# Optimization experiments

Measured on AMD Instinct MI355X. Metric: run time of the kernel, lower is better.

## Reference

```python
import jax, jax.numpy as jnp
import numpy as np


def setup_inputs() -> dict:
    key = jax.random.key(0)
    k1, _ = jax.random.split(key)
    x = jax.random.normal(k1, (8, 128, 56, 56), dtype=jnp.float32)
    gamma = jnp.array(0.5, dtype=jnp.float32)  # learned scalar (init gamma=0.5)
    return {"x": x, "gamma": gamma}


def reference(x, gamma):
    # conv=False path: query/key/value convs are Identity, so Q=K=V=x flattened.
    B, C, H, W = x.shape
    N = H * W
    v = x.reshape(B, C, N)                          # [B, C, N]
    # energy[b, i, j] = sum_c x[b, c, i] * x[b, c, j]  (Q^T K)
    energy = jnp.einsum('bci,bcj->bij', v, v)       # [B, N, N]
    # multiplicative mask: zero out the diagonal BEFORE softmax (not -inf)
    mask = 1.0 - jnp.eye(N, dtype=energy.dtype)
    attention = jax.nn.softmax(energy * mask, axis=-1)  # [B, N, N]
    # out = bmm(V, attention): out[b, c, j] = sum_i v[b, c, i] * attention[b, i, j]
    out = jnp.einsum('bci,bij->bcj', v, attention)  # [B, C, N]
    out = jax.nn.relu(out).reshape(B, C, H, W)
    y = gamma * out + x
    return (y, out, x, gamma)
```

## Files before the change

kernel.cpp:

```cpp
#include <hip/hip_runtime.h>
#include <math.h>

#define Bb 8
#define Cc 128
#define Nn 3136
#define Np 3200
#define NT 50
#define Mm (Bb*Cc*Nn)
#define PADV 72
#define L2E 1.44269504088896340736f
#define C44 (44.0f * L2E)

#define XT2B (NT*16*64*8)
#define XC2B (NT*8*128*8)

typedef unsigned short u16;
typedef __attribute__((ext_vector_type(8)))  u16      u16x8;
typedef __attribute__((ext_vector_type(8)))  _Float16 f16x8;
typedef __attribute__((ext_vector_type(4)))  _Float16 f16x4;
typedef __attribute__((ext_vector_type(4)))  float    f32x4;
typedef __attribute__((ext_vector_type(16))) float    f32x16;

__device__ __forceinline__ float exp2fast(float x) {
#if __has_builtin(__builtin_amdgcn_exp2f)
    return __builtin_amdgcn_exp2f(x);
#else
    float r; asm volatile("v_exp_f32 %0, %1" : "=v"(r) : "v"(x)); return r;
#endif
}

__global__ __launch_bounds__(256) void prep_kernel(const float* __restrict__ x,
                                                   const float* __restrict__ gamma_p,
                                                   float* __restrict__ out,
                                                   u16* __restrict__ xt2,
                                                   u16* __restrict__ xc2,
                                                   float* __restrict__ row_d) {
    const int bx = blockIdx.x;
    const int b = bx / 50, nblk = bx % 50;
    const int t = threadIdx.x;

    if (nblk == 49) {
        const u16x8 z8 = {0, 0, 0, 0, 0, 0, 0, 0};
        u16* dt = xt2 + ((size_t)b * NT + 49) * (16 * 64 * 8);
        u16* dc = xc2 + ((size_t)b * NT + 49) * (8 * 128 * 8);
        #pragma unroll
        for (int it = 0; it < 4; ++it) {
            *(u16x8*)&dt[(it * 256 + t) * 8] = z8;
            *(u16x8*)&dc[(it * 256 + t) * 8] = z8;
        }
        if (t < 64) row_d[b * Np + Nn + t] = 1.0f;
        return;
    }

    __shared__ float lx[Cc][65];
    const int n0 = nblk * 64;

    #pragma unroll 8
    for (int r = 0; r < 32; ++r) {
        const int c = r * 4 + (t >> 6);
        const int g = (b * Cc + c) * Nn + n0 + (t & 63);
        const float v = x[g];
        lx[c][t & 63] = v;
        out[(size_t)2 * Mm + g] = v;
    }
    __syncthreads();

    {
        const int nl = t & 63, cseg = t >> 6;
        u16x8 hv[4];
        #pragma unroll
        for (int cc = 0; cc < 32; ++cc) {
            const _Float16 hh = (_Float16)lx[cseg * 32 + cc][nl];
            hv[cc >> 3][cc & 7] = __builtin_bit_cast(u16, hh);
        }
        u16* base = xt2 + (((size_t)(b * NT + nblk) * 16 + cseg * 4) * 64 + nl) * 8;
        #pragma unroll
        for (int k = 0; k < 4; ++k) *(u16x8*)&base[k * (64 * 8)] = hv[k];
    }
    {
        const int c = t >> 1, half = t & 1;
        u16x8 hv[4];
        #pragma unroll
        for (int k = 0; k < 32; ++k) {
            const _Float16 hh = (_Float16)lx[c][half * 32 + k];
            hv[k >> 3][k & 7] = __builtin_bit_cast(u16, hh);
        }
        u16* base = xc2 + (((size_t)(b * NT + nblk) * 8 + half * 4) * 128 + c) * 8;
        #pragma unroll
        for (int k = 0; k < 4; ++k) *(u16x8*)&base[k * (128 * 8)] = hv[k];
    }
    if (bx == 0 && t == 0) out[(size_t)3 * Mm] = gamma_p[0];
}

__global__ __launch_bounds__(256, 5) void stats_kernel(const u16* __restrict__ xt2,
                                                       float* __restrict__ row_d) {
    const int bx = blockIdx.x;
    const int b = bx & 7, rem = bx >> 3;
    const int i0t = rem >> 2, jq = rem & 3;
    const int t = threadIdx.x;
    const int w = t >> 6, l = t & 63, lane = l & 31, h = l >> 5;
    const int igrp = w & 1, jsub = w >> 1;
    const u16* __restrict__ xb = xt2 + (size_t)b * XT2B;

    f16x8 Bf[8];
    const int irow = igrp * 32 + lane;
    #pragma unroll
    for (int kk = 0; kk < 8; ++kk)
        Bf[kk] = *(const f16x8*)&xb[(((size_t)i0t * 16 + 2 * kk + h) * 64 + irow) * 8];

    float sa = 0.f, sb = 0.f;
    const int jt0 = jq * 12 + (jq < 2 ? jq : 2);
    const int jcnt = 12 + (jq < 2 ? 1 : 0);
    const int jrow = jsub * 32 + lane;

    for (int jt = jt0; jt < jt0 + jcnt; ++jt) {
        const u16* ab = &xb[((size_t)jt * 16 * 64 + jrow) * 8];
        f32x16 acc;
        #pragma unroll
        for (int r = 0; r < 16; ++r) acc[r] = 0.f;
        #pragma unroll
        for (int kk = 0; kk < 8; ++kk) {
            const f16x8 A = *(const f16x8*)&ab[(2 * kk + h) * 512];
            acc = __builtin_amdgcn_mfma_f32_32x32x16_f16(A, Bf[kk], acc, 0, 0, 0);
        }
        if (jt == i0t) {
            const bool dsub = (jsub == igrp);
            #pragma unroll
            for (int r = 0; r < 16; ++r) {
                const int mrow = (r & 3) + 8 * (r >> 2) + 4 * h;
                float v = acc[r];
                if (dsub && mrow == lane) v = 0.f;
                const float e = exp2fast(fmaf(v, L2E, -C44));
                if (r & 1) sb += e; else sa += e;
            }
        } else {
            #pragma unroll
            for (int r = 0; r < 16; ++r) {
                const float e = exp2fast(fmaf(acc[r], L2E, -C44));
                if (r & 1) sb += e; else sa += e;
            }
        }
    }
    float ssum = sa + sb;
    ssum += __shfl_xor(ssum, 32, 64);
    if (h == 0) atomicAdd(&row_d[b * Np + i0t * 64 + igrp * 32 + lane], ssum);
}

__global__ __launch_bounds__(256) void conv_kernel(float* __restrict__ row_d) {
    const int i = blockIdx.x * 256 + threadIdx.x;
    row_d[i] = C44 + __log2f(row_d[i]);
}

__global__ __launch_bounds__(256, 3) void out_kernel(const u16* __restrict__ xt2,
                                                     const u16* __restrict__ xc2,
                                                     const float* __restrict__ row_c,
                                                     float* __restrict__ out) {
    __shared__ u16 s_pt[2][64 * PADV];

    const int bx = blockIdx.x;
    const int b = bx & 7, rem = bx >> 3;
    const int j0t = rem >> 1, ih = rem & 1;
    const int t = threadIdx.x;
    const int w = t >> 6, l = t & 63, lane = l & 31, h = l >> 5;
    const int isub = w & 1, jgrp = w >> 1;
    const int jg = w & 1,  cp = w >> 1;
    const u16* __restrict__ xtb = xt2 + (size_t)b * XT2B;
    const u16* __restrict__ xcb = xc2 + (size_t)b * XC2B;

    f16x8 Bj[8];
    const int jrow = jgrp * 32 + lane;
    #pragma unroll
    for (int kk = 0; kk < 8; ++kk)
        Bj[kk] = *(const f16x8*)&xtb[(((size_t)j0t * 16 + 2 * kk + h) * 64 + jrow) * 8];

    f32x16 oa, ob;
    #pragma unroll
    for (int r = 0; r < 16; ++r) { oa[r] = 0.f; ob[r] = 0.f; }

    const int arow = isub * 32 + lane;
    const int ptbase = (jgrp * 32 + lane) * PADV + isub * 32;
    const int pbrow = (jg * 32 + lane) * PADV + h * 8;

    for (int ti = ih * 25; ti < ih * 25 + 25; ++ti) {
        f32x16 ea;
        #pragma unroll
        for (int r = 0; r < 16; ++r) ea[r] = 0.f;
        const u16* ab = &xtb[((size_t)ti * 16 * 64 + arow) * 8];
        #pragma unroll
        for (int kk = 0; kk < 8; ++kk) {
            const f16x8 A = *(const f16x8*)&ab[(2 * kk + h) * 512];
            ea = __builtin_amdgcn_mfma_f32_32x32x16_f16(A, Bj[kk], ea, 0, 0, 0);
        }

        u16* pt = &s_pt[ti & 1][0];
        const float* cbase = &row_c[b * Np + ti * 64 + isub * 32];
        if (ti == j0t) {
            const bool dsub = (isub == jgrp);
            #pragma unroll
            for (int q = 0; q < 4; ++q) {
                const f32x4 cv = *(const f32x4*)&cbase[q * 8 + h * 4];
                f16x4 pv;
                #pragma unroll
                for (int r = 0; r < 4; ++r) {
                    const int m = q * 8 + h * 4 + r;
                    float v = ea[q * 4 + r];
                    if (dsub && m == lane) v = 0.f;
                    pv[r] = (_Float16)exp2fast(fmaf(v, L2E, -cv[r]));
                }
                *(f16x4*)&pt[ptbase + q * 8 + h * 4] = pv;
            }
        } else {
            #pragma unroll
            for (int q = 0; q < 4; ++q) {
                const f32x4 cv = *(const f32x4*)&cbase[q * 8 + h * 4];
                f16x4 pv;
                #pragma unroll
                for (int r = 0; r < 4; ++r)
                    pv[r] = (_Float16)exp2fast(fmaf(ea[q * 4 + r], L2E, -cv[r]));
                *(f16x4*)&pt[ptbase + q * 8 + h * 4] = pv;
            }
        }
        __syncthreads();

        const u16* vb = &xcb[((size_t)ti * 8 * 128 + cp * 64 + lane) * 8];
        #pragma unroll
        for (int kk = 0; kk < 4; ++kk) {
            const f16x8 Bp  = *(const f16x8*)&pt[pbrow + kk * 16];
            const f16x8 Av0 = *(const f16x8*)&vb[((2 * kk + h) * 128) * 8];
            const f16x8 Av1 = *(const f16x8*)&vb[((2 * kk + h) * 128 + 32) * 8];
            oa = __builtin_amdgcn_mfma_f32_32x32x16_f16(Av0, Bp, oa, 0, 0, 0);
            ob = __builtin_amdgcn_mfma_f32_32x32x16_f16(Av1, Bp, ob, 0, 0, 0);
        }
    }

    #pragma unroll
    for (int r = 0; r < 16; ++r) {
        const int mrow = (r & 3) + 8 * (r >> 2) + 4 * h;
        const int jj = j0t * 64 + jg * 32 + lane;
        {
            const int c = cp * 64 + mrow;
            const size_t pos = (size_t)(b * Cc + c) * Nn + jj;
            out[(size_t)ih * Mm + pos] = oa[r];
        }
        {
            const int c = cp * 64 + 32 + mrow;
            const size_t pos = (size_t)(b * Cc + c) * Nn + jj;
            out[(size_t)ih * Mm + pos] = ob[r];
        }
    }
}

__global__ __launch_bounds__(256) void finish_kernel(const float* __restrict__ x,
                                                     const float* __restrict__ gamma_p,
                                                     float* __restrict__ out) {
    const float gamma = gamma_p[0];
    const size_t base = ((size_t)blockIdx.x * 256 + threadIdx.x) * 4;
    const f32x4 pa = *(const f32x4*)&out[base];
    const f32x4 pb = *(const f32x4*)&out[(size_t)Mm + base];
    const f32x4 xv = *(const f32x4*)&x[base];
    f32x4 yo, oo;
    #pragma unroll
    for (int r = 0; r < 4; ++r) {
        const float o = fmaxf(pa[r] + pb[r], 0.0f);
        oo[r] = o;
        yo[r] = fmaf(gamma, o, xv[r]);
    }
    *(f32x4*)&out[base] = yo;
    *(f32x4*)&out[(size_t)Mm + base] = oo;
}

extern "C" void kernel_launch(void* const* d_in, const int* in_sizes, int n_in,
                              void* d_out, int out_size, void* d_ws, size_t ws_size,
                              hipStream_t stream) {
    const float* x       = (const float*)d_in[0];
    const float* gamma_p = (const float*)d_in[1];
    float* out = (float*)d_out;

    float* row_d = (float*)d_ws;
    u16* xt2 = (u16*)((char*)d_ws + (1 << 17));
    u16* xc2 = xt2 + (size_t)Bb * XT2B;

    hipMemsetAsync(row_d, 0, (size_t)Bb * Np * sizeof(float), stream);
    prep_kernel  <<<400, 256, 0, stream>>>(x, gamma_p, out, xt2, xc2, row_d);
    stats_kernel <<<1568, 256, 0, stream>>>(xt2, row_d);
    conv_kernel  <<<100, 256, 0, stream>>>(row_d);
    out_kernel   <<<784, 256, 0, stream>>>(xt2, xc2, row_d, out);
    finish_kernel<<<3136, 256, 0, stream>>>(x, gamma_p, out);
}
```

Measured before the change: 190.9 us.

## Keep softmax probabilities in registers, split key range three ways, prefetch stats tiles

The out kernel no longer stages probability tiles through shared memory with a barrier each step. It packs them to fp16 in registers and uses cross-lane shuffles to build the MFMA B operand directly. Each wave now accumulates all 128 channels, and partial sums from the two i-subgroups are reduced once through shared memory at the end. The i-range is split into three partitions instead of two to expose more blocks, and the finish kernel now sums three partials and writes the x copy that prep used to write. Separately, the stats kernel double-buffers its A-tile loads and uses two accumulator chains with setprio hints, at the cost of more registers and lower occupancy bounds.

```diff
diff --git a/kernel.cpp b/kernel.cpp
--- a/kernel.cpp
+++ b/kernel.cpp
@@ -7,7 +7,6 @@
 #define Np 3200
 #define NT 50
 #define Mm (Bb*Cc*Nn)
-#define PADV 72
 #define L2E 1.44269504088896340736f
 #define C44 (44.0f * L2E)
 
@@ -15,9 +14,11 @@
 #define XC2B (NT*8*128*8)
 
 typedef unsigned short u16;
+typedef unsigned int   u32;
 typedef __attribute__((ext_vector_type(8)))  u16      u16x8;
 typedef __attribute__((ext_vector_type(8)))  _Float16 f16x8;
-typedef __attribute__((ext_vector_type(4)))  _Float16 f16x4;
+typedef __attribute__((ext_vector_type(2)))  _Float16 f16x2;
+typedef __attribute__((ext_vector_type(4)))  u32      u32x4;
 typedef __attribute__((ext_vector_type(4)))  float    f32x4;
 typedef __attribute__((ext_vector_type(16))) float    f32x16;
 
@@ -25,7 +26,7 @@
 #if __has_builtin(__builtin_amdgcn_exp2f)
     return __builtin_amdgcn_exp2f(x);
 #else
-    float r; asm volatile("v_exp_f32 %0, %1" : "=v"(r) : "v"(x)); return r;
+    float r; asm("v_exp_f32 %0, %1" : "=v"(r) : "v"(x)); return r;
 #endif
 }
 
@@ -59,9 +60,7 @@
     for (int r = 0; r < 32; ++r) {
         const int c = r * 4 + (t >> 6);
         const int g = (b * Cc + c) * Nn + n0 + (t & 63);
-        const float v = x[g];
-        lx[c][t & 63] = v;
-        out[(size_t)2 * Mm + g] = v;
+        lx[c][t & 63] = x[g];
     }
     __syncthreads();
 
@@ -92,7 +91,7 @@
     if (bx == 0 && t == 0) out[(size_t)3 * Mm] = gamma_p[0];
 }
 
-__global__ __launch_bounds__(256, 5) void stats_kernel(const u16* __restrict__ xt2,
+__global__ __launch_bounds__(256, 3) void stats_kernel(const u16* __restrict__ xt2,
                                                        float* __restrict__ row_d) {
     const int bx = blockIdx.x;
     const int b = bx & 7, rem = bx >> 3;
@@ -108,27 +107,43 @@
     for (int kk = 0; kk < 8; ++kk)
         Bf[kk] = *(const f16x8*)&xb[(((size_t)i0t * 16 + 2 * kk + h) * 64 + irow) * 8];
 
-    float sa = 0.f, sb = 0.f;
     const int jt0 = jq * 12 + (jq < 2 ? jq : 2);
     const int jcnt = 12 + (jq < 2 ? 1 : 0);
     const int jrow = jsub * 32 + lane;
 
+    f16x8 Ac[8], An[8];
+    {
+        const u16* ab = &xb[((size_t)jt0 * 16 * 64 + jrow) * 8];
+        #pragma unroll
+        for (int kk = 0; kk < 8; ++kk)
+            Ac[kk] = *(const f16x8*)&ab[(2 * kk + h) * 512];
+    }
+
+    float sa = 0.f, sb = 0.f;
     for (int jt = jt0; jt < jt0 + jcnt; ++jt) {
-        const u16* ab = &xb[((size_t)jt * 16 * 64 + jrow) * 8];
-        f32x16 acc;
-        #pragma unroll
-        for (int r = 0; r < 16; ++r) acc[r] = 0.f;
-        #pragma unroll
-        for (int kk = 0; kk < 8; ++kk) {
-            const f16x8 A = *(const f16x8*)&ab[(2 * kk + h) * 512];
-            acc = __builtin_amdgcn_mfma_f32_32x32x16_f16(A, Bf[kk], acc, 0, 0, 0);
-        }
+        const int tn = (jt + 1 < jt0 + jcnt) ? jt + 1 : jt;
+        const u16* an = &xb[((size_t)tn * 16 * 64 + jrow) * 8];
+        #pragma unroll
+        for (int kk = 0; kk < 8; ++kk)
+            An[kk] = *(const f16x8*)&an[(2 * kk + h) * 512];
+
+        f32x16 ea, eb;
+        #pragma unroll
+        for (int r = 0; r < 16; ++r) { ea[r] = 0.f; eb[r] = 0.f; }
+        __builtin_amdgcn_s_setprio(1);
+        #pragma unroll
+        for (int kk = 0; kk < 4; ++kk) {
+            ea = __builtin_amdgcn_mfma_f32_32x32x16_f16(Ac[2 * kk],     Bf[2 * kk],     ea, 0, 0, 0);
+            eb = __builtin_amdgcn_mfma_f32_32x32x16_f16(Ac[2 * kk + 1], Bf[2 * kk + 1], eb, 0, 0, 0);
+        }
+        __builtin_amdgcn_s_setprio(0);
+
         if (jt == i0t) {
             const bool dsub = (jsub == igrp);
             #pragma unroll
             for (int r = 0; r < 16; ++r) {
                 const int mrow = (r & 3) + 8 * (r >> 2) + 4 * h;
-                float v = acc[r];
+                float v = ea[r] + eb[r];
                 if (dsub && mrow == lane) v = 0.f;
                 const float e = exp2fast(fmaf(v, L2E, -C44));
                 if (r & 1) sb += e; else sa += e;
@@ -136,10 +151,12 @@
         } else {
             #pragma unroll
             for (int r = 0; r < 16; ++r) {
-                const float e = exp2fast(fmaf(acc[r], L2E, -C44));
+                const float e = exp2fast(fmaf(ea[r] + eb[r], L2E, -C44));
                 if (r & 1) sb += e; else sa += e;
             }
         }
+        #pragma unroll
+        for (int kk = 0; kk < 8; ++kk) Ac[kk] = An[kk];
     }
     float ssum = sa + sb;
     ssum += __shfl_xor(ssum, 32, 64);
@@ -151,19 +168,20 @@
     row_d[i] = C44 + __log2f(row_d[i]);
 }
 
-__global__ __launch_bounds__(256, 3) void out_kernel(const u16* __restrict__ xt2,
+__global__ __launch_bounds__(256, 2) void out_kernel(const u16* __restrict__ xt2,
                                                      const u16* __restrict__ xc2,
                                                      const float* __restrict__ row_c,
                                                      float* __restrict__ out) {
-    __shared__ u16 s_pt[2][64 * PADV];
+    __shared__ float sred[2][4][16][64];
 
     const int bx = blockIdx.x;
     const int b = bx & 7, rem = bx >> 3;
-    const int j0t = rem >> 1, ih = rem & 1;
+    const int j0t = rem / 3, q = rem % 3;
+    const int ti0 = (q == 0) ? 0 : (q == 1 ? 17 : 34);
+    const int ti1 = (q == 0) ? 17 : (q == 1 ? 34 : 50);
     const int t = threadIdx.x;
     const int w = t >> 6, l = t & 63, lane = l & 31, h = l >> 5;
     const int isub = w & 1, jgrp = w >> 1;
-    const int jg = w & 1,  cp = w >> 1;
     const u16* __restrict__ xtb = xt2 + (size_t)b * XT2B;
     const u16* __restrict__ xcb = xc2 + (size_t)b * XC2B;
 
@@ -173,79 +191,95 @@
     for (int kk = 0; kk < 8; ++kk)
         Bj[kk] = *(const f16x8*)&xtb[(((size_t)j0t * 16 + 2 * kk + h) * 64 + jrow) * 8];
 
-    f32x16 oa, ob;
+    f32x16 acc[4];
     #pragma unroll
-    for (int r = 0; r < 16; ++r) { oa[r] = 0.f; ob[r] = 0.f; }
+    for (int ct = 0; ct < 4; ++ct)
+        #pragma unroll
+        for (int r = 0; r < 16; ++r) acc[ct][r] = 0.f;
 
     const int arow = isub * 32 + lane;
-    const int ptbase = (jgrp * 32 + lane) * PADV + isub * 32;
-    const int pbrow = (jg * 32 + lane) * PADV + h * 8;
-
-    for (int ti = ih * 25; ti < ih * 25 + 25; ++ti) {
+
+    for (int ti = ti0; ti < ti1; ++ti) {
+        f16x8 Ae[8];
+        const u16* ab = &xtb[((size_t)ti * 16 * 64 + arow) * 8];
+        #pragma unroll
+        for (int kk = 0; kk < 8; ++kk)
+            Ae[kk] = *(const f16x8*)&ab[(2 * kk + h) * 512];
+
+        f16x8 Av[4][2];
+        const u16* vb = &xcb[((size_t)(ti * 8 + isub * 4 + h) * 128 + lane) * 8];
+        #pragma unroll
+        for (int ct = 0; ct < 4; ++ct)
+            #pragma unroll
+            for (int kt = 0; kt < 2; ++kt)
+                Av[ct][kt] = *(const f16x8*)&vb[kt * 2 * 1024 + ct * 256];
+
         f32x16 ea;
         #pragma unroll
         for (int r = 0; r < 16; ++r) ea[r] = 0.f;
-        const u16* ab = &xtb[((size_t)ti * 16 * 64 + arow) * 8];
-        #pragma unroll
-        for (int kk = 0; kk < 8; ++kk) {
-            const f16x8 A = *(const f16x8*)&ab[(2 * kk + h) * 512];
-            ea = __builtin_amdgcn_mfma_f32_32x32x16_f16(A, Bj[kk], ea, 0, 0, 0);
-        }
-
-        u16* pt = &s_pt[ti & 1][0];
-        const float* cbase = &row_c[b * Np + ti * 64 + isub * 32];
-        if (ti == j0t) {
-            const bool dsub = (isub == jgrp);
-            #pragma unroll
-            for (int q = 0; q < 4; ++q) {
-                const f32x4 cv = *(const f32x4*)&cbase[q * 8 + h * 4];
-                f16x4 pv;
-                #pragma unroll
-                for (int r = 0; r < 4; ++r) {
-                    const int m = q * 8 + h * 4 + r;
-                    float v = ea[q * 4 + r];
-                    if (dsub && m == lane) v = 0.f;
-                    pv[r] = (_Float16)exp2fast(fmaf(v, L2E, -cv[r]));
-                }
-                *(f16x4*)&pt[ptbase + q * 8 + h * 4] = pv;
+        __builtin_amdgcn_s_setprio(1);
+        #pragma unroll
+        for (int kk = 0; kk < 8; ++kk)
+            ea = __builtin_amdgcn_mfma_f32_32x32x16_f16(Ae[kk], Bj[kk], ea, 0, 0, 0);
+        __builtin_amdgcn_s_setprio(0);
+
+        const float* cb = &row_c[b * Np + ti * 64 + isub * 32];
+        const bool dt = (ti == j0t) && (isub == jgrp);
+        u32 pk[4][2], sw[4][2];
+        #pragma unroll
+        for (int qq = 0; qq < 4; ++qq) {
+            const f32x4 cv = *(const f32x4*)&cb[qq * 8 + h * 4];
+            float pv[4];
+            #pragma unroll
+            for (int r2 = 0; r2 < 4; ++r2) {
+                const int m = qq * 8 + h * 4 + r2;
+                float v = ea[qq * 4 + r2];
+                if (dt && m == lane) v = 0.f;
+                pv[r2] = exp2fast(fmaf(v, L2E, -cv[r2]));
             }
-        } else {
-            #pragma unroll
-            for (int q = 0; q < 4; ++q) {
-                const f32x4 cv = *(const f32x4*)&cbase[q * 8 + h * 4];
-                f16x4 pv;
-                #pragma unroll
-                for (int r = 0; r < 4; ++r)
-                    pv[r] = (_Float16)exp2fast(fmaf(ea[q * 4 + r], L2E, -cv[r]));
-                *(f16x4*)&pt[ptbase + q * 8 + h * 4] = pv;
+            pk[qq][0] = __builtin_bit_cast(u32, __builtin_amdgcn_cvt_pkrtz(pv[0], pv[1]));
+            pk[qq][1] = __builtin_bit_cast(u32, __builtin_amdgcn_cvt_pkrtz(pv[2], pv[3]));
+            sw[qq][0] = __shfl_xor(pk[qq][0], 32, 64);
+            sw[qq][1] = __shfl_xor(pk[qq][1], 32, 64);
+        }
+        f16x8 Bp[2];
+        #pragma unroll
+        for (int kt = 0; kt < 2; ++kt) {
+            u32x4 bw;
+            bw[0] = h ? sw[2 * kt + 1][0] : pk[2 * kt][0];
+            bw[1] = h ? sw[2 * kt + 1][1] : pk[2 * kt][1];
+            bw[2] = h ? pk[2 * kt + 1][0] : sw[2 * kt][0];
+            bw[3] = h ? pk[2 * kt + 1][1] : sw[2 * kt][1];
+            Bp[kt] = __builtin_bit_cast(f16x8, bw);
+        }
+
+        __builtin_amdgcn_s_setprio(1);
+        #pragma unroll
+        for (int ct = 0; ct < 4; ++ct)
+            #pragma unroll
+            for (int kt = 0; kt < 2; ++kt)
+                acc[ct] = __builtin_amdgcn_mfma_f32_32x32x16_f16(Av[ct][kt], Bp[kt], acc[ct], 0, 0, 0);
+        __builtin_amdgcn_s_setprio(0);
+    }
+
+    if (isub == 1) {
+        #pragma unroll
+        for (int ct = 0; ct < 4; ++ct)
+            #pragma unroll
+            for (int r = 0; r < 16; ++r)
+                sred[jgrp][ct][r][l] = acc[ct][r];
+    }
+    __syncthreads();
+    if (isub == 0) {
+        const int jj = j0t * 64 + jgrp * 32 + lane;
+        #pragma unroll
+        for (int ct = 0; ct < 4; ++ct) {
+            #pragma unroll
+            for (int r = 0; r < 16; ++r) {
+                const int mrow = (r & 3) + 8 * (r >> 2) + 4 * h;
+                const float v = acc[ct][r] + sred[jgrp][ct][r][l];
+                out[(size_t)q * Mm + (size_t)(b * Cc + ct * 32 + mrow) * Nn + jj] = v;
             }
-        }
-        __syncthreads();
-
-        const u16* vb = &xcb[((size_t)ti * 8 * 128 + cp * 64 + lane) * 8];
-        #pragma unroll
-        for (int kk = 0; kk < 4; ++kk) {
-            const f16x8 Bp  = *(const f16x8*)&pt[pbrow + kk * 16];
-            const f16x8 Av0 = *(const f16x8*)&vb[((2 * kk + h) * 128) * 8];
-            const f16x8 Av1 = *(const f16x8*)&vb[((2 * kk + h) * 128 + 32) * 8];
-            oa = __builtin_amdgcn_mfma_f32_32x32x16_f16(Av0, Bp, oa, 0, 0, 0);
-            ob = __builtin_amdgcn_mfma_f32_32x32x16_f16(Av1, Bp, ob, 0, 0, 0);
-        }
-    }
-
-    #pragma unroll
-    for (int r = 0; r < 16; ++r) {
-        const int mrow = (r & 3) + 8 * (r >> 2) + 4 * h;
-        const int jj = j0t * 64 + jg * 32 + lane;
-        {
-            const int c = cp * 64 + mrow;
-            const size_t pos = (size_t)(b * Cc + c) * Nn + jj;
-            out[(size_t)ih * Mm + pos] = oa[r];
-        }
-        {
-            const int c = cp * 64 + 32 + mrow;
-            const size_t pos = (size_t)(b * Cc + c) * Nn + jj;
-            out[(size_t)ih * Mm + pos] = ob[r];
         }
     }
 }
@@ -257,16 +291,18 @@
     const size_t base = ((size_t)blockIdx.x * 256 + threadIdx.x) * 4;
     const f32x4 pa = *(const f32x4*)&out[base];
     const f32x4 pb = *(const f32x4*)&out[(size_t)Mm + base];
+    const f32x4 pc = *(const f32x4*)&out[(size_t)2 * Mm + base];
     const f32x4 xv = *(const f32x4*)&x[base];
     f32x4 yo, oo;
     #pragma unroll
     for (int r = 0; r < 4; ++r) {
-        const float o = fmaxf(pa[r] + pb[r], 0.0f);
+        const float o = fmaxf(pa[r] + pb[r] + pc[r], 0.0f);
         oo[r] = o;
         yo[r] = fmaf(gamma, o, xv[r]);
     }
     *(f32x4*)&out[base] = yo;
     *(f32x4*)&out[(size_t)Mm + base] = oo;
+    *(f32x4*)&out[(size_t)2 * Mm + base] = xv;
 }
 
 extern "C" void kernel_launch(void* const* d_in, const int* in_sizes, int n_in,
@@ -284,6 +320,6 @@
     prep_kernel  <<<400, 256, 0, stream>>>(x, gamma_p, out, xt2, xc2, row_d);
     stats_kernel <<<1568, 256, 0, stream>>>(xt2, row_d);
     conv_kernel  <<<100, 256, 0, stream>>>(row_d);
-    out_kernel   <<<784, 256, 0, stream>>>(xt2, xc2, row_d, out);
+    out_kernel   <<<1176, 256, 0, stream>>>(xt2, xc2, row_d, out);
     finish_kernel<<<3136, 256, 0, stream>>>(x, gamma_p, out);
 }
```

New measurement: 201.5 us. +5.6%, slower.

## Split attention kernels three ways, dual-accumulator MFMA chains, and setprio

Applied to the files above, without the earlier changes.

The out kernel now splits the i-range into three partial sums instead of two. It uses the x-copy output slot as the third partial buffer, and the finish kernel sums three partials and writes x afterward. The stats kernel splits each row's j-range eight ways instead of four, doubling the grid. Both kernels break the MFMA dependency chain into two independent accumulators, raise wave priority around MFMA sections, and out_kernel targets higher occupancy. The aim is more parallelism and shorter MFMA latency chains, at the cost of more atomics, extra partial-buffer traffic and more register pressure.

```diff
diff --git a/kernel.cpp b/kernel.cpp
--- a/kernel.cpp
+++ b/kernel.cpp
@@ -15,6 +15,7 @@
 #define XC2B (NT*8*128*8)
 
 typedef unsigned short u16;
+typedef unsigned int   u32;
 typedef __attribute__((ext_vector_type(8)))  u16      u16x8;
 typedef __attribute__((ext_vector_type(8)))  _Float16 f16x8;
 typedef __attribute__((ext_vector_type(4)))  _Float16 f16x4;
@@ -25,7 +26,7 @@
 #if __has_builtin(__builtin_amdgcn_exp2f)
     return __builtin_amdgcn_exp2f(x);
 #else
-    float r; asm volatile("v_exp_f32 %0, %1" : "=v"(r) : "v"(x)); return r;
+    float r; asm("v_exp_f32 %0, %1" : "=v"(r) : "v"(x)); return r;
 #endif
 }
 
@@ -59,9 +60,7 @@
     for (int r = 0; r < 32; ++r) {
         const int c = r * 4 + (t >> 6);
         const int g = (b * Cc + c) * Nn + n0 + (t & 63);
-        const float v = x[g];
-        lx[c][t & 63] = v;
-        out[(size_t)2 * Mm + g] = v;
+        lx[c][t & 63] = x[g];
     }
     __syncthreads();
 
@@ -96,7 +95,7 @@
                                                        float* __restrict__ row_d) {
     const int bx = blockIdx.x;
     const int b = bx & 7, rem = bx >> 3;
-    const int i0t = rem >> 2, jq = rem & 3;
+    const int i0t = rem >> 3, jq = rem & 7;
     const int t = threadIdx.x;
     const int w = t >> 6, l = t & 63, lane = l & 31, h = l >> 5;
     const int igrp = w & 1, jsub = w >> 1;
@@ -108,27 +107,32 @@
     for (int kk = 0; kk < 8; ++kk)
         Bf[kk] = *(const f16x8*)&xb[(((size_t)i0t * 16 + 2 * kk + h) * 64 + irow) * 8];
 
+    const int jt0 = jq * 6 + (jq < 2 ? jq : 2);
+    const int jcnt = 6 + (jq < 2 ? 1 : 0);
+    const int jrow = jsub * 32 + lane;
+
     float sa = 0.f, sb = 0.f;
-    const int jt0 = jq * 12 + (jq < 2 ? jq : 2);
-    const int jcnt = 12 + (jq < 2 ? 1 : 0);
-    const int jrow = jsub * 32 + lane;
-
     for (int jt = jt0; jt < jt0 + jcnt; ++jt) {
         const u16* ab = &xb[((size_t)jt * 16 * 64 + jrow) * 8];
-        f32x16 acc;
-        #pragma unroll
-        for (int r = 0; r < 16; ++r) acc[r] = 0.f;
-        #pragma unroll
-        for (int kk = 0; kk < 8; ++kk) {
-            const f16x8 A = *(const f16x8*)&ab[(2 * kk + h) * 512];
-            acc = __builtin_amdgcn_mfma_f32_32x32x16_f16(A, Bf[kk], acc, 0, 0, 0);
-        }
+        f32x16 ea, eb;
+        #pragma unroll
+        for (int r = 0; r < 16; ++r) { ea[r] = 0.f; eb[r] = 0.f; }
+        __builtin_amdgcn_s_setprio(1);
+        #pragma unroll
+        for (int kk = 0; kk < 4; ++kk) {
+            const f16x8 A0 = *(const f16x8*)&ab[(4 * kk + h) * 512];
+            const f16x8 A1 = *(const f16x8*)&ab[(4 * kk + 2 + h) * 512];
+            ea = __builtin_amdgcn_mfma_f32_32x32x16_f16(A0, Bf[2 * kk],     ea, 0, 0, 0);
+            eb = __builtin_amdgcn_mfma_f32_32x32x16_f16(A1, Bf[2 * kk + 1], eb, 0, 0, 0);
+        }
+        __builtin_amdgcn_s_setprio(0);
+
         if (jt == i0t) {
             const bool dsub = (jsub == igrp);
             #pragma unroll
             for (int r = 0; r < 16; ++r) {
                 const int mrow = (r & 3) + 8 * (r >> 2) + 4 * h;
-                float v = acc[r];
+                float v = ea[r] + eb[r];
                 if (dsub && mrow == lane) v = 0.f;
                 const float e = exp2fast(fmaf(v, L2E, -C44));
                 if (r & 1) sb += e; else sa += e;
@@ -136,7 +140,7 @@
         } else {
             #pragma unroll
             for (int r = 0; r < 16; ++r) {
-                const float e = exp2fast(fmaf(acc[r], L2E, -C44));
+                const float e = exp2fast(fmaf(ea[r] + eb[r], L2E, -C44));
                 if (r & 1) sb += e; else sa += e;
             }
         }
@@ -151,7 +155,7 @@
     row_d[i] = C44 + __log2f(row_d[i]);
 }
 
-__global__ __launch_bounds__(256, 3) void out_kernel(const u16* __restrict__ xt2,
+__global__ __launch_bounds__(256, 4) void out_kernel(const u16* __restrict__ xt2,
                                                      const u16* __restrict__ xc2,
                                                      const float* __restrict__ row_c,
                                                      float* __restrict__ out) {
@@ -159,7 +163,9 @@
 
     const int bx = blockIdx.x;
     const int b = bx & 7, rem = bx >> 3;
-    const int j0t = rem >> 1, ih = rem & 1;
+    const int j0t = rem / 3, q = rem % 3;
+    const int ti0 = q * 17;
+    const int ti1 = (q == 2) ? 50 : ti0 + 17;
     const int t = threadIdx.x;
     const int w = t >> 6, l = t & 63, lane = l & 31, h = l >> 5;
     const int isub = w & 1, jgrp = w >> 1;
@@ -181,48 +187,54 @@
     const int ptbase = (jgrp * 32 + lane) * PADV + isub * 32;
     const int pbrow = (jg * 32 + lane) * PADV + h * 8;
 
-    for (int ti = ih * 25; ti < ih * 25 + 25; ++ti) {
-        f32x16 ea;
-        #pragma unroll
-        for (int r = 0; r < 16; ++r) ea[r] = 0.f;
+    for (int ti = ti0; ti < ti1; ++ti) {
+        f32x16 ea, eb;
+        #pragma unroll
+        for (int r = 0; r < 16; ++r) { ea[r] = 0.f; eb[r] = 0.f; }
         const u16* ab = &xtb[((size_t)ti * 16 * 64 + arow) * 8];
-        #pragma unroll
-        for (int kk = 0; kk < 8; ++kk) {
-            const f16x8 A = *(const f16x8*)&ab[(2 * kk + h) * 512];
-            ea = __builtin_amdgcn_mfma_f32_32x32x16_f16(A, Bj[kk], ea, 0, 0, 0);
-        }
+        __builtin_amdgcn_s_setprio(1);
+        #pragma unroll
+        for (int kk = 0; kk < 4; ++kk) {
+            const f16x8 A0 = *(const f16x8*)&ab[(4 * kk + h) * 512];
+            const f16x8 A1 = *(const f16x8*)&ab[(4 * kk + 2 + h) * 512];
+            ea = __builtin_amdgcn_mfma_f32_32x32x16_f16(A0, Bj[2 * kk],     ea, 0, 0, 0);
+            eb = __builtin_amdgcn_mfma_f32_32x32x16_f16(A1, Bj[2 * kk + 1], eb, 0, 0, 0);
+        }
+        __builtin_amdgcn_s_setprio(0);
 
         u16* pt = &s_pt[ti & 1][0];
         const float* cbase = &row_c[b * Np + ti * 64 + isub * 32];
         if (ti == j0t) {
             const bool dsub = (isub == jgrp);
             #pragma unroll
-            for (int q = 0; q < 4; ++q) {
-                const f32x4 cv = *(const f32x4*)&cbase[q * 8 + h * 4];
+            for (int qq = 0; qq < 4; ++qq) {
+                const f32x4 cv = *(const f32x4*)&cbase[qq * 8 + h * 4];
                 f16x4 pv;
                 #pragma unroll
                 for (int r = 0; r < 4; ++r) {
-                    const int m = q * 8 + h * 4 + r;
-                    float v = ea[q * 4 + r];
+                    const int m = qq * 8 + h * 4 + r;
+                    float v = ea[qq * 4 + r] + eb[qq * 4 + r];
                     if (dsub && m == lane) v = 0.f;
                     pv[r] = (_Float16)exp2fast(fmaf(v, L2E, -cv[r]));
                 }
-                *(f16x4*)&pt[ptbase + q * 8 + h * 4] = pv;
+                *(f16x4*)&pt[ptbase + qq * 8 + h * 4] = pv;
             }
         } else {
             #pragma unroll
-            for (int q = 0; q < 4; ++q) {
-                const f32x4 cv = *(const f32x4*)&cbase[q * 8 + h * 4];
+            for (int qq = 0; qq < 4; ++qq) {
+                const f32x4 cv = *(const f32x4*)&cbase[qq * 8 + h * 4];
                 f16x4 pv;
                 #pragma unroll
                 for (int r = 0; r < 4; ++r)
-                    pv[r] = (_Float16)exp2fast(fmaf(ea[q * 4 + r], L2E, -cv[r]));
-                *(f16x4*)&pt[ptbase + q * 8 + h * 4] = pv;
+                    pv[r] = (_Float16)exp2fast(
+                        fmaf(ea[qq * 4 + r] + eb[qq * 4 + r], L2E, -cv[r]));
+                *(f16x4*)&pt[ptbase + qq * 8 + h * 4] = pv;
             }
         }
         __syncthreads();
 
         const u16* vb = &xcb[((size_t)ti * 8 * 128 + cp * 64 + lane) * 8];
+        __builtin_amdgcn_s_setprio(1);
         #pragma unroll
         for (int kk = 0; kk < 4; ++kk) {
             const f16x8 Bp  = *(const f16x8*)&pt[pbrow + kk * 16];
@@ -231,6 +243,7 @@
             oa = __builtin_amdgcn_mfma_f32_32x32x16_f16(Av0, Bp, oa, 0, 0, 0);
             ob = __builtin_amdgcn_mfma_f32_32x32x16_f16(Av1, Bp, ob, 0, 0, 0);
         }
+        __builtin_amdgcn_s_setprio(0);
     }
 
     #pragma unroll
@@ -240,12 +253,12 @@
         {
             const int c = cp * 64 + mrow;
             const size_t pos = (size_t)(b * Cc + c) * Nn + jj;
-            out[(size_t)ih * Mm + pos] = oa[r];
+            out[(size_t)q * Mm + pos] = oa[r];
         }
         {
             const int c = cp * 64 + 32 + mrow;
             const size_t pos = (size_t)(b * Cc + c) * Nn + jj;
-            out[(size_t)ih * Mm + pos] = ob[r];
+            out[(size_t)q * Mm + pos] = ob[r];
         }
     }
 }
@@ -257,16 +270,18 @@
     const size_t base = ((size_t)blockIdx.x * 256 + threadIdx.x) * 4;
     const f32x4 pa = *(const f32x4*)&out[base];
     const f32x4 pb = *(const f32x4*)&out[(size_t)Mm + base];
+    const f32x4 pc = *(const f32x4*)&out[(size_t)2 * Mm + base];
     const f32x4 xv = *(const f32x4*)&x[base];
     f32x4 yo, oo;
     #pragma unroll
     for (int r = 0; r < 4; ++r) {
-        const float o = fmaxf(pa[r] + pb[r], 0.0f);
+        const float o = fmaxf(pa[r] + pb[r] + pc[r], 0.0f);
         oo[r] = o;
         yo[r] = fmaf(gamma, o, xv[r]);
     }
     *(f32x4*)&out[base] = yo;
     *(f32x4*)&out[(size_t)Mm + base] = oo;
+    *(f32x4*)&out[(size_t)2 * Mm + base] = xv;
 }
 
 extern "C" void kernel_launch(void* const* d_in, const int* in_sizes, int n_in,
@@ -282,8 +297,8 @@
 
     hipMemsetAsync(row_d, 0, (size_t)Bb * Np * sizeof(float), stream);
     prep_kernel  <<<400, 256, 0, stream>>>(x, gamma_p, out, xt2, xc2, row_d);
-    stats_kernel <<<1568, 256, 0, stream>>>(xt2, row_d);
+    stats_kernel <<<3136, 256, 0, stream>>>(xt2, row_d);
     conv_kernel  <<<100, 256, 0, stream>>>(row_d);
-    out_kernel   <<<784, 256, 0, stream>>>(xt2, xc2, row_d, out);
+    out_kernel   <<<1176, 256, 0, stream>>>(xt2, xc2, row_d, out);
     finish_kernel<<<3136, 256, 0, stream>>>(x, gamma_p, out);
 }
```

Result: slower. 212.3 us (+11.2%).
